# Kernel optimization log

Measured on AMD Instinct MI355X. Metric: run time of the kernel, lower is better.

The kernel has to match this reference:

```python
import jax, jax.numpy as jnp
import numpy as np

B, L, C, EW, H = 4, 512, 512, 64, 8
D = C // H          # dot_dim = 64
NI = 1024           # node ffn inner = round(512*2.0)
EI = 64             # edge ffn inner = round(64*1.0)
CLIP_LO, CLIP_HI = -5.0, 5.0


def _ln(x, g, b):
    m = jnp.mean(x, -1, keepdims=True)
    v = jnp.var(x, -1, keepdims=True)
    return (x - m) * jax.lax.rsqrt(v + 1e-5) * g + b


def setup_inputs() -> dict:
    key = jax.random.key(0)
    ks = iter(jax.random.split(key, 16))
    nrm = lambda shp: (0.02 * jax.random.normal(next(ks), shp)).astype(jnp.float32)
    z = lambda n: jnp.zeros((n,), jnp.float32)
    o = lambda n: jnp.ones((n,), jnp.float32)
    return {
        'h': jax.random.normal(next(ks), (B, L, C), jnp.float32),
        'e': jax.random.normal(next(ks), (B, L, L, EW), jnp.float32),
        'ln_h_g': o(C), 'ln_h_b': z(C),
        'ln_e_g': o(EW), 'ln_e_b': z(EW),
        'W_QKV': nrm((C, 3 * C)), 'b_QKV': z(3 * C),
        'W_E': nrm((EW, H)), 'b_E': z(H),
        'W_G': nrm((EW, H)), 'b_G': z(H),
        'W_Oh': nrm((C, C)), 'b_Oh': z(C),
        'ffn_ln_h_g': o(C), 'ffn_ln_h_b': z(C),
        'W_h1': nrm((C, NI)), 'b_h1': z(NI),
        'W_h2': nrm((NI, C)), 'b_h2': z(C),
        'W_Oe': nrm((H, EW)), 'b_Oe': z(EW),
        'ffn_ln_e_g': o(EW), 'ffn_ln_e_b': z(EW),
        'W_e1': nrm((EW, EI)), 'b_e1': z(EI),
        'W_e2': nrm((EI, EW)), 'b_e2': z(EW),
    }


def reference(h, e, ln_h_g, ln_h_b, ln_e_g, ln_e_b, W_QKV, b_QKV, W_E, b_E,
              W_G, b_G, W_Oh, b_Oh, ffn_ln_h_g, ffn_ln_h_b, W_h1, b_h1,
              W_h2, b_h2, W_Oe, b_Oe, ffn_ln_e_g, ffn_ln_e_b, W_e1, b_e1,
              W_e2, b_e2):
    h_ln = _ln(h, ln_h_g, ln_h_b)
    e_ln = _ln(e, ln_e_g, ln_e_b)
    QKV = h_ln @ W_QKV + b_QKV                    # [B,L,3C]
    E = e_ln @ W_E + b_E                          # [B,L,L,H]
    G = e_ln @ W_G + b_G                          # [B,L,L,H]
    qkv = QKV.reshape(B, L, 3 * D, H)             # torch view(B,L,-1,H)
    Q, K, V = qkv[:, :, :D], qkv[:, :, D:2 * D], qkv[:, :, 2 * D:]
    A_hat = jnp.einsum('bldh,bmdh->blmh', Q, K) * (D ** -0.5)
    H_hat = jnp.clip(A_hat, CLIP_LO, CLIP_HI) + E  # [B,L,L,H]
    gates = jax.nn.sigmoid(G)
    A_tild = jax.nn.softmax(H_hat, axis=2) * gates
    V_att = jnp.einsum('blmh,bmkh->blkh', A_tild, V)  # [B,L,D,H]
    deg = jnp.log1p(jnp.sum(gates, axis=2, keepdims=True))  # [B,L,1,H]
    V_att = (V_att * deg).reshape(B, L, C)
    # node MHA residual + FFN
    h1 = V_att @ W_Oh + b_Oh + h
    h_f = _ln(h1, ffn_ln_h_g, ffn_ln_h_b)
    h_out = h1 + (jax.nn.elu(h_f @ W_h1 + b_h1) @ W_h2 + b_h2)
    # edge MHA residual + FFN
    e1 = H_hat @ W_Oe + b_Oe + e
    e_f = _ln(e1, ffn_ln_e_g, ffn_ln_e_b)
    e_out = e1 + (jax.nn.elu(e_f @ W_e1 + b_e1) @ W_e2 + b_e2)
    return (h_out, e_out)
```

## Files before the change

kernel.cpp:

```cpp
#include <hip/hip_runtime.h>
#include <math.h>

typedef unsigned short u16t;
typedef unsigned int   u32t;
typedef __bf16 bf16x2 __attribute__((ext_vector_type(2)));
typedef __bf16 bf16x8 __attribute__((ext_vector_type(8)));
typedef float  f32x4  __attribute__((ext_vector_type(4)));

#define DEV static __device__ __forceinline__

DEV u16t bfc(float x){ __bf16 b = (__bf16)x; return __builtin_bit_cast(u16t, b); }
DEV u32t pkbf(float a, float b){ bf16x2 v = {(__bf16)a, (__bf16)b}; return __builtin_bit_cast(u32t, v); }
DEV float flc(u16t u){ return __uint_as_float(((u32t)u)<<16); }
DEV u32t pk2(u16t a, u16t b){ return (u32t)a | ((u32t)b<<16); }
DEV f32x4 fz4(){ f32x4 z = {0.f,0.f,0.f,0.f}; return z; }
DEV bf16x8 bz8(){ uint4 z = make_uint4(0u,0u,0u,0u); return __builtin_bit_cast(bf16x8, z); }
DEV f32x4 MFMA(bf16x8 a, bf16x8 b, f32x4 c){ return __builtin_amdgcn_mfma_f32_16x16x32_bf16(a,b,c,0,0,0); }

__global__ void kwTall(const float* __restrict__ A, u16t* __restrict__ oA,
                       const float* __restrict__ B, u16t* __restrict__ oB,
                       const float* __restrict__ C, u16t* __restrict__ oC,
                       const float* __restrict__ D, u16t* __restrict__ oD){
  int id = blockIdx.x*256 + threadIdx.x;
  if (id < 786432){ int n=id>>9, k=id&511; oA[id]=bfc(A[(size_t)k*1536+n]); return; }
  id -= 786432;
  if (id < 262144){ int n=id>>9, k=id&511; int ks=(k&63)*8+(k>>6); oB[id]=bfc(B[(size_t)ks*512+n]); return; }
  id -= 262144;
  if (id < 524288){ int n=id>>9, k=id&511; oC[id]=bfc(C[(size_t)k*1024+n]); return; }
  id -= 524288;
  { int n=id>>10, k=id&1023; oD[id]=bfc(D[(size_t)k*512+n]); }
}

__global__ __launch_bounds__(256) void kln(const float* __restrict__ in, const float* __restrict__ g,
                                           const float* __restrict__ b, u16t* __restrict__ out){
  int wv = threadIdx.x >> 6, lane = threadIdx.x & 63;
  int row = blockIdx.x*4 + wv;
  const float4* rp = reinterpret_cast<const float4*>(in + (size_t)row*512);
  float4 v0 = rp[lane], v1 = rp[lane+64];
  float s = v0.x+v0.y+v0.z+v0.w + v1.x+v1.y+v1.z+v1.w;
  float q = v0.x*v0.x+v0.y*v0.y+v0.z*v0.z+v0.w*v0.w + v1.x*v1.x+v1.y*v1.y+v1.z*v1.z+v1.w*v1.w;
  #pragma unroll
  for (int m=1;m<64;m<<=1){ s += __shfl_xor(s,m); q += __shfl_xor(q,m); }
  float mean = s*(1.f/512.f), var = q*(1.f/512.f)-mean*mean, rs = rsqrtf(var+1e-5f);
  const float4* gp = reinterpret_cast<const float4*>(g);
  const float4* bp = reinterpret_cast<const float4*>(b);
  float4 g0=gp[lane], g1=gp[lane+64], b0=bp[lane], b1=bp[lane+64];
  u16t* op = out + (size_t)row*512;
  uint2 o0, o1;
  o0.x = pkbf((v0.x-mean)*rs*g0.x+b0.x, (v0.y-mean)*rs*g0.y+b0.y);
  o0.y = pkbf((v0.z-mean)*rs*g0.z+b0.z, (v0.w-mean)*rs*g0.w+b0.w);
  o1.x = pkbf((v1.x-mean)*rs*g1.x+b1.x, (v1.y-mean)*rs*g1.y+b1.y);
  o1.y = pkbf((v1.z-mean)*rs*g1.z+b1.z, (v1.w-mean)*rs*g1.w+b1.w);
  reinterpret_cast<uint2*>(op)[lane]    = o0;
  reinterpret_cast<uint2*>(op)[lane+64] = o1;
}

__global__ __launch_bounds__(256) void kqkv(const u16t* __restrict__ hln, const u16t* __restrict__ Wt,
    const float* __restrict__ bias, u16t* __restrict__ Qb, u16t* __restrict__ Kb, u16t* __restrict__ Vt)
{
  __shared__ __align__(16) u16t As[16][520];
  __shared__ __align__(16) u16t Cs[16][1024];
  const int r0 = blockIdx.x*16, t = threadIdx.x;
  const int b8 = (r0 >> 9) * 8, pos0 = r0 & 511;
  {
    int row = t>>4, seg = t&15;
    const uint4* src = reinterpret_cast<const uint4*>(hln + (size_t)(r0+row)*512 + seg*32);
    uint4* dst = reinterpret_cast<uint4*>(&As[row][seg*32]);
    dst[0]=src[0]; dst[1]=src[1]; dst[2]=src[2]; dst[3]=src[3];
  }
  __syncthreads();
  const int wv = t>>6, lane = t&63;
  const int frow = lane&15, kgrp = (lane>>4)*8, rbase = (lane>>4)*4;
  for (int nt=0; nt<24; nt++){
    int n0 = (wv*24+nt)*16;
    f32x4 acc = fz4();
    for (int k0=0;k0<512;k0+=32){
      bf16x8 af = *reinterpret_cast<const bf16x8*>(&As[frow][k0+kgrp]);
      bf16x8 bf_ = *reinterpret_cast<const bf16x8*>(Wt + (size_t)(n0+frow)*512 + k0+kgrp);
      acc = MFMA(af,bf_,acc);
    }
    int col = n0 + frow;
    float bs = bias[col];
    if (n0 < 1024){
      #pragma unroll
      for (int r=0;r<4;r++) Cs[rbase+r][col] = bfc(acc[r]+bs);
    } else {
      int cc = col - 1024, dv = cc>>3, hq = cc&7;
      ushort4 u4 = make_ushort4(bfc(acc[0]+bs), bfc(acc[1]+bs), bfc(acc[2]+bs), bfc(acc[3]+bs));
      *reinterpret_cast<ushort4*>(Vt + ((size_t)(b8+hq)*64 + dv)*512 + pos0 + rbase) = u4;
    }
  }
  __syncthreads();
  {
    int pair = t>>1, halfq = t&1;
    int hq = pair>>4, lq = pair&15, d0 = halfq*32;
    int pos = pos0 + lq;
    u16t* qdst = Qb + ((size_t)(b8+hq)*512 + pos)*64 + d0;
    u16t* kdst = Kb + ((size_t)(b8+hq)*512 + pos)*64 + d0;
    #pragma unroll
    for (int v2=0; v2<4; v2++){
      uint4 u, uk;
      u.x  = pk2(Cs[lq][(d0+v2*8+0)*8+hq], Cs[lq][(d0+v2*8+1)*8+hq]);
      u.y  = pk2(Cs[lq][(d0+v2*8+2)*8+hq], Cs[lq][(d0+v2*8+3)*8+hq]);
      u.z  = pk2(Cs[lq][(d0+v2*8+4)*8+hq], Cs[lq][(d0+v2*8+5)*8+hq]);
      u.w  = pk2(Cs[lq][(d0+v2*8+6)*8+hq], Cs[lq][(d0+v2*8+7)*8+hq]);
      uk.x = pk2(Cs[lq][512+(d0+v2*8+0)*8+hq], Cs[lq][512+(d0+v2*8+1)*8+hq]);
      uk.y = pk2(Cs[lq][512+(d0+v2*8+2)*8+hq], Cs[lq][512+(d0+v2*8+3)*8+hq]);
      uk.z = pk2(Cs[lq][512+(d0+v2*8+4)*8+hq], Cs[lq][512+(d0+v2*8+5)*8+hq]);
      uk.w = pk2(Cs[lq][512+(d0+v2*8+6)*8+hq], Cs[lq][512+(d0+v2*8+7)*8+hq]);
      reinterpret_cast<uint4*>(qdst)[v2] = u;
      reinterpret_cast<uint4*>(kdst)[v2] = uk;
    }
  }
}

__global__ __launch_bounds__(512,4) void kattnF(
    const float* __restrict__ e, const float* __restrict__ lng, const float* __restrict__ lnb,
    const float* __restrict__ WE, const float* __restrict__ bE,
    const float* __restrict__ WG, const float* __restrict__ bG,
    const u16t* __restrict__ Qb, const u16t* __restrict__ Kb, const u16t* __restrict__ Vt,
    const float* __restrict__ WOe, const float* __restrict__ bOe,
    const float* __restrict__ flg, const float* __restrict__ flb,
    const float* __restrict__ We1, const float* __restrict__ be1,
    const float* __restrict__ We2, const float* __restrict__ be2,
    u16t* __restrict__ Vp, float* __restrict__ Sp, float* __restrict__ Dp,
    float* __restrict__ eout)
{
  __shared__ __align__(16) u16t Eln[256][72];
  __shared__ u16t EGb[256][18];
  __shared__ __align__(16) u16t Hl[256][8];
  __shared__ __align__(16) u16t Pgs[16][8][16];
  __shared__ __align__(16) u16t WEGt[16][72];
  __shared__ __align__(16) u16t We1t[64][72];
  __shared__ __align__(16) u16t We2t[64][72];
  __shared__ __align__(16) u16t WOeT[64][8];
  __shared__ float lgs[64], lbs[64], flgs[64], flbs[64], bOes[64], be1s[64], be2s[64];
  __shared__ float bEs[8], bGs[8];

  const int t = threadIdx.x;
  const int b = blockIdx.z, lblk = blockIdx.x, chunk = blockIdx.y;
  const int l0 = lblk*16, m0g = chunk*128, b8 = b*8;

  if (t < 64){
    lgs[t]=lng[t]; lbs[t]=lnb[t]; flgs[t]=flg[t]; flbs[t]=flb[t];
    bOes[t]=bOe[t]; be1s[t]=be1[t]; be2s[t]=be2[t];
  }
  if (t < 8){ bEs[t]=bE[t]; bGs[t]=bG[t]; }
  for (int i=t; i<1024; i+=512){
    int n = i>>6, k = i&63;
    WEGt[n][k] = bfc(n<8 ? WE[k*8+n] : WG[k*8+(n-8)]);
  }
  for (int i=t; i<4096; i+=512){
    int n=i>>6, k=i&63;
    We1t[n][k] = bfc(We1[k*64+n]);
    We2t[n][k] = bfc(We2[k*64+n]);
  }
  {
    int n=t>>3, hh=t&7;
    WOeT[n][hh] = bfc(WOe[hh*64+n]);
  }
  __syncthreads();

  const int wv = t>>6, lane = t&63;
  const int frow = lane&15, kgrp = (lane>>4)*8, rbase = (lane>>4)*4;

  bf16x8 qf[2];
  #pragma unroll
  for (int kk=0;kk<2;kk++)
    qf[kk] = *reinterpret_cast<const bf16x8*>(Qb + ((size_t)(b8+wv)*512 + l0+frow)*64 + kk*32 + kgrp);

  float Ssum[4] = {0.f,0.f,0.f,0.f}, Dsum[4] = {0.f,0.f,0.f,0.f};
  f32x4 accV[4];
  #pragma unroll
  for (int d=0;d<4;d++) accV[d]=fz4();

  const float* ebs[2];
  #pragma unroll
  for (int ti=0; ti<2; ti++)
    ebs[ti] = e + ((size_t)((b*512 + l0 + 2*wv+ti)*512) + m0g + frow)*64 + rbase;

  float4 xr[2][4];
  #pragma unroll
  for (int ti=0; ti<2; ti++)
    #pragma unroll
    for (int nb=0; nb<4; nb++)
      xr[ti][nb] = *reinterpret_cast<const float4*>(ebs[ti] + nb*16);

  #pragma unroll 1
  for (int mt=0; mt<8; mt++){
    const int m0 = m0g + mt*16;
    #pragma unroll
    for (int ti=0; ti<2; ti++){
      const int T = 2*wv + ti;
      float s_=0.f, q_=0.f;
      #pragma unroll
      for (int nb=0; nb<4; nb++){
        float4 v = xr[ti][nb];
        s_ += v.x+v.y+v.z+v.w;
        q_ += v.x*v.x+v.y*v.y+v.z*v.z+v.w*v.w;
      }
      s_ += __shfl_xor(s_,16); q_ += __shfl_xor(q_,16);
      s_ += __shfl_xor(s_,32); q_ += __shfl_xor(q_,32);
      float mean = s_*(1.f/64.f), var = q_*(1.f/64.f)-mean*mean, rs = rsqrtf(var+1e-5f);
      #pragma unroll
      for (int nb=0; nb<4; nb++){
        int n = nb*16 + rbase;
        float4 v = xr[ti][nb];
        uint2 uv;
        uv.x = pkbf((v.x-mean)*rs*lgs[n  ]+lbs[n  ], (v.y-mean)*rs*lgs[n+1]+lbs[n+1]);
        uv.y = pkbf((v.z-mean)*rs*lgs[n+2]+lbs[n+2], (v.w-mean)*rs*lgs[n+3]+lbs[n+3]);
        *reinterpret_cast<uint2*>(&Eln[T*16+frow][n]) = uv;
      }
    }
    #pragma unroll
    for (int ti=0; ti<2; ti++){
      int T = wv*2+ti;
      bf16x8 a0 = *reinterpret_cast<const bf16x8*>(&Eln[T*16+frow][kgrp]);
      bf16x8 a1 = *reinterpret_cast<const bf16x8*>(&Eln[T*16+frow][32+kgrp]);
      bf16x8 w0 = *reinterpret_cast<const bf16x8*>(&WEGt[frow][kgrp]);
      bf16x8 w1 = *reinterpret_cast<const bf16x8*>(&WEGt[frow][32+kgrp]);
      f32x4 acc = fz4(); acc = MFMA(a0,w0,acc); acc = MFMA(a1,w1,acc);
      #pragma unroll
      for (int r=0;r<4;r++) EGb[T*16+rbase+r][frow] = bfc(acc[r]);
    }
    __syncthreads();
    {
      const u16t* kb = Kb + ((size_t)(b8+wv)*512 + m0)*64 + frow*64 + kgrp;
      bf16x8 kf0 = *reinterpret_cast<const bf16x8*>(kb);
      bf16x8 kf1 = *reinterpret_cast<const bf16x8*>(kb + 32);
      f32x4 aq = fz4();
      aq = MFMA(qf[0], kf0, aq);
      aq = MFMA(qf[1], kf1, aq);
      #pragma unroll
      for (int r=0;r<4;r++){
        int lrow = rbase + r;
        int eidx = lrow*16 + frow;
        float ah = aq[r]*0.125f;
        ah = fminf(fmaxf(ah, -5.f), 5.f);
        float Ev = flc(EGb[eidx][wv])   + bEs[wv];
        float Gv = flc(EGb[eidx][8+wv]) + bGs[wv];
        float Hv = ah + Ev;
        float P = __expf(Hv);
        float g = 1.f/(1.f+__expf(-Gv));
        Ssum[r] += P; Dsum[r] += g;
        Hl[eidx][wv] = bfc(Hv);
        Pgs[lrow][wv][frow] = bfc(P*g);
      }
    }
    {
      bf16x8 pa = (kgrp<16)
        ? *reinterpret_cast<const bf16x8*>(&Pgs[frow][wv][kgrp]) : bz8();
      #pragma unroll
      for (int db=0; db<4; db++){
        bf16x8 vb = (kgrp<16)
          ? *reinterpret_cast<const bf16x8*>(Vt + ((size_t)(b8+wv)*64 + db*16+frow)*512 + m0 + kgrp)
          : bz8();
        accV[db] = MFMA(pa, vb, accV[db]);
      }
    }
    __syncthreads();
    #pragma unroll
    for (int ti=0; ti<2; ti++){
      const int T = 2*wv + ti;
      bf16x8 hf_ = bz8();
      if (kgrp==0) hf_ = *reinterpret_cast<const bf16x8*>(&Hl[T*16+frow][0]);
      f32x4 e1a[4];
      #pragma unroll
      for (int nb=0; nb<4; nb++){
        bf16x8 wf = bz8();
        if (kgrp==0) wf = *reinterpret_cast<const bf16x8*>(&WOeT[nb*16][0] + frow*8);
        e1a[nb] = MFMA(wf, hf_, fz4());
      }
      #pragma unroll
      for (int nb=0; nb<4; nb++){
        int n = nb*16 + rbase;
        e1a[nb][0] += bOes[n  ] + xr[ti][nb].x;
        e1a[nb][1] += bOes[n+1] + xr[ti][nb].y;
        e1a[nb][2] += bOes[n+2] + xr[ti][nb].z;
        e1a[nb][3] += bOes[n+3] + xr[ti][nb].w;
      }
      if (mt+1 < 8){
        #pragma unroll
        for (int nb=0; nb<4; nb++)
          xr[ti][nb] = *reinterpret_cast<const float4*>(ebs[ti] + (size_t)(mt+1)*1024 + nb*16);
      }
      {
        float s_=0.f, q_=0.f;
        #pragma unroll
        for (int nb=0; nb<4; nb++){
          #pragma unroll
          for (int r=0;r<4;r++){ float v = e1a[nb][r]; s_ += v; q_ += v*v; }
        }
        s_ += __shfl_xor(s_,16); q_ += __shfl_xor(q_,16);
        s_ += __shfl_xor(s_,32); q_ += __shfl_xor(q_,32);
        float mean = s_*(1.f/64.f), var = q_*(1.f/64.f)-mean*mean, rs = rsqrtf(var+1e-5f);
        #pragma unroll
        for (int nb=0; nb<4; nb++){
          int n = nb*16 + rbase;
          uint2 uv;
          uv.x = pkbf((e1a[nb][0]-mean)*rs*flgs[n  ]+flbs[n  ], (e1a[nb][1]-mean)*rs*flgs[n+1]+flbs[n+1]);
          uv.y = pkbf((e1a[nb][2]-mean)*rs*flgs[n+2]+flbs[n+2], (e1a[nb][3]-mean)*rs*flgs[n+3]+flbs[n+3]);
          *reinterpret_cast<uint2*>(&Eln[T*16+frow][n]) = uv;
        }
      }
      {
        bf16x8 x0 = *reinterpret_cast<const bf16x8*>(&Eln[T*16+frow][kgrp]);
        bf16x8 x1 = *reinterpret_cast<const bf16x8*>(&Eln[T*16+frow][32+kgrp]);
        f32x4 acc1[4];
        #pragma unroll
        for (int nb=0;nb<4;nb++){
          bf16x8 w0 = *reinterpret_cast<const bf16x8*>(&We1t[nb*16+frow][kgrp]);
          bf16x8 w1 = *reinterpret_cast<const bf16x8*>(&We1t[nb*16+frow][32+kgrp]);
          f32x4 a_ = fz4(); a_ = MFMA(w0,x0,a_); a_ = MFMA(w1,x1,a_);
          acc1[nb] = a_;
        }
        #pragma unroll
        for (int nb=0;nb<4;nb++){
          int n = nb*16 + rbase;
          float v0 = acc1[nb][0] + be1s[n  ]; v0 = v0>0.f ? v0 : (__expf(v0)-1.f);
          float v1 = acc1[nb][1] + be1s[n+1]; v1 = v1>0.f ? v1 : (__expf(v1)-1.f);
          float v2 = acc1[nb][2] + be1s[n+2]; v2 = v2>0.f ? v2 : (__expf(v2)-1.f);
          float v3 = acc1[nb][3] + be1s[n+3]; v3 = v3>0.f ? v3 : (__expf(v3)-1.f);
          uint2 uv;
          uv.x = pkbf(v0, v1);
          uv.y = pkbf(v2, v3);
          *reinterpret_cast<uint2*>(&Eln[T*16+frow][n]) = uv;
        }
      }
      {
        bf16x8 x0 = *reinterpret_cast<const bf16x8*>(&Eln[T*16+frow][kgrp]);
        bf16x8 x1 = *reinterpret_cast<const bf16x8*>(&Eln[T*16+frow][32+kgrp]);
        float* eob = eout + ((size_t)((b*512 + l0 + T)*512) + m0 + frow)*64 + rbase;
        #pragma unroll
        for (int nb=0;nb<4;nb++){
          bf16x8 w0 = *reinterpret_cast<const bf16x8*>(&We2t[nb*16+frow][kgrp]);
          bf16x8 w1 = *reinterpret_cast<const bf16x8*>(&We2t[nb*16+frow][32+kgrp]);
          f32x4 a_ = fz4(); a_ = MFMA(w0,x0,a_); a_ = MFMA(w1,x1,a_);
          int n = nb*16 + rbase;
          float4 o;
          o.x = a_[0] + be2s[n  ] + e1a[nb][0];
          o.y = a_[1] + be2s[n+1] + e1a[nb][1];
          o.z = a_[2] + be2s[n+2] + e1a[nb][2];
          o.w = a_[3] + be2s[n+3] + e1a[nb][3];
          *reinterpret_cast<float4*>(eob + nb*16) = o;
        }
      }
    }
  }

  #pragma unroll
  for (int r=0;r<4;r++){
    float sv = Ssum[r], dv = Dsum[r];
    #pragma unroll
    for (int msk=1; msk<16; msk<<=1){ sv += __shfl_xor(sv, msk); dv += __shfl_xor(dv, msk); }
    int lrow = rbase + r;
    if (frow == 0){
      size_t idx = ((size_t)(b*512 + l0 + lrow)*8 + wv)*4 + chunk;
      Sp[idx] = sv; Dp[idx] = dv;
    }
  }
  __syncthreads();
  float* Vo = reinterpret_cast<float*>(&Eln[0][0]);
  #pragma unroll
  for (int db=0; db<4; db++){
    #pragma unroll
    for (int r=0;r<4;r++)
      Vo[(size_t)(rbase+r)*512 + wv*64 + db*16 + frow] = accV[db][r];
  }
  __syncthreads();
  {
    int row = t>>5, i = t&31;
    u16t* vpb = Vp + ((size_t)(chunk*2048 + b*512 + l0 + row))*512 + i*16;
    const float* vsrc = &Vo[(size_t)row*512 + i*16];
    uint4 o0, o1;
    o0.x = pkbf(vsrc[0],  vsrc[1]);  o0.y = pkbf(vsrc[2],  vsrc[3]);
    o0.z = pkbf(vsrc[4],  vsrc[5]);  o0.w = pkbf(vsrc[6],  vsrc[7]);
    o1.x = pkbf(vsrc[8],  vsrc[9]);  o1.y = pkbf(vsrc[10], vsrc[11]);
    o1.z = pkbf(vsrc[12], vsrc[13]); o1.w = pkbf(vsrc[14], vsrc[15]);
    reinterpret_cast<uint4*>(vpb)[0] = o0;
    reinterpret_cast<uint4*>(vpb)[1] = o1;
  }
}

__global__ __launch_bounds__(256) void kvfin(const u16t* __restrict__ Vp,
    const float* __restrict__ Sp, const float* __restrict__ Dp, u16t* __restrict__ Va)
{
  const int row = blockIdx.x;
  const int t = threadIdx.x;
  __shared__ float scl[8];
  if (t < 8){
    const float* sp = Sp + ((size_t)row*8 + t)*4;
    const float* dp = Dp + ((size_t)row*8 + t)*4;
    float S = sp[0]+sp[1]+sp[2]+sp[3];
    float D = dp[0]+dp[1]+dp[2]+dp[3];
    scl[t] = log1pf(D)/S;
  }
  __syncthreads();
  int c = t*2;
  float v0=0.f, v1=0.f;
  #pragma unroll
  for (int ch=0; ch<4; ch++){
    u32t u = *reinterpret_cast<const u32t*>(Vp + ((size_t)(ch*2048 + row))*512 + c);
    v0 += flc((u16t)(u & 0xffffu));
    v1 += flc((u16t)(u >> 16));
  }
  float s = scl[c>>6];
  *reinterpret_cast<u32t*>(Va + (size_t)row*512 + c) = pkbf(v0*s, v1*s);
}

__global__ __launch_bounds__(256) void kgemmNS(const u16t* __restrict__ A, const u16t* __restrict__ Bt,
    const float* __restrict__ bias, const float* __restrict__ res,
    float* __restrict__ outf, u16t* __restrict__ outb, int N, int K, int do_elu)
{
  __shared__ __align__(16) u16t As[16][1032];
  const int r0 = blockIdx.x*16, t = threadIdx.x;
  {
    int row = t>>4, seg = t&15, cnt = K>>4;
    const uint4* src = reinterpret_cast<const uint4*>(A + (size_t)(r0+row)*K + seg*cnt);
    uint4* dst = reinterpret_cast<uint4*>(&As[row][seg*cnt]);
    for (int i=0;i<(cnt>>3);i++) dst[i] = src[i];
  }
  __syncthreads();
  const int wv = t>>6, lane = t&63;
  const int frow = lane&15, kgrp = (lane>>4)*8, rbase = (lane>>4)*4;
  int n0 = (blockIdx.y*4 + wv)*16;
  f32x4 acc = fz4();
  for (int k0=0;k0<K;k0+=32){
    bf16x8 af = *reinterpret_cast<const bf16x8*>(&As[frow][k0+kgrp]);
    bf16x8 bf_ = *reinterpret_cast<const bf16x8*>(Bt + (size_t)(n0+frow)*K + k0+kgrp);
    acc = MFMA(af,bf_,acc);
  }
  int col = n0 + frow;
  float bs = bias[col];
  #pragma unroll
  for (int r=0;r<4;r++){
    size_t row = (size_t)(r0 + rbase + r);
    float v = acc[r] + bs;
    if (do_elu) v = v>0.f ? v : (__expf(v)-1.f);
    if (res)  v += res[row*N + col];
    if (outf) outf[row*N + col] = v;
    if (outb) outb[row*N + col] = bfc(v);
  }
}

extern "C" void kernel_launch(void* const* d_in, const int* in_sizes, int n_in,
                              void* d_out, int out_size, void* d_ws, size_t ws_size,
                              hipStream_t stream)
{
  (void)in_sizes; (void)n_in; (void)out_size; (void)ws_size;
  const float* h      = (const float*)d_in[0];
  const float* e      = (const float*)d_in[1];
  const float* ln_h_g = (const float*)d_in[2];
  const float* ln_h_b = (const float*)d_in[3];
  const float* ln_e_g = (const float*)d_in[4];
  const float* ln_e_b = (const float*)d_in[5];
  const float* W_QKV  = (const float*)d_in[6];
  const float* b_QKV  = (const float*)d_in[7];
  const float* W_E    = (const float*)d_in[8];
  const float* b_E    = (const float*)d_in[9];
  const float* W_G    = (const float*)d_in[10];
  const float* b_G    = (const float*)d_in[11];
  const float* W_Oh   = (const float*)d_in[12];
  const float* b_Oh   = (const float*)d_in[13];
  const float* f_ln_h_g = (const float*)d_in[14];
  const float* f_ln_h_b = (const float*)d_in[15];
  const float* W_h1   = (const float*)d_in[16];
  const float* b_h1   = (const float*)d_in[17];
  const float* W_h2   = (const float*)d_in[18];
  const float* b_h2   = (const float*)d_in[19];
  const float* W_Oe   = (const float*)d_in[20];
  const float* b_Oe   = (const float*)d_in[21];
  const float* f_ln_e_g = (const float*)d_in[22];
  const float* f_ln_e_b = (const float*)d_in[23];
  const float* W_e1   = (const float*)d_in[24];
  const float* b_e1   = (const float*)d_in[25];
  const float* W_e2   = (const float*)d_in[26];
  const float* b_e2   = (const float*)d_in[27];

  float* out   = (float*)d_out;
  float* h_out = out;
  float* e_out = out + (size_t)4*512*512;

  char* w = (char*)d_ws;
  size_t off = 0;
  auto alloc = [&](size_t bytes)->char*{ char* p = w + off; off += (bytes + 255) & ~(size_t)255; return p; };
  u16t* hln   = (u16t*)alloc(2048ull*512*2);
  u16t* WtQKV = (u16t*)alloc(1536ull*512*2);
  u16t* WtOh  = (u16t*)alloc(512ull*512*2);
  u16t* WtH1  = (u16t*)alloc(1024ull*512*2);
  u16t* WtH2  = (u16t*)alloc(512ull*1024*2);
  u16t* Qb    = (u16t*)alloc(4ull*8*512*64*2);
  u16t* Kb    = (u16t*)alloc(4ull*8*512*64*2);
  u16t* Vt    = (u16t*)alloc(4ull*8*64*512*2);
  u16t* Vp    = (u16t*)alloc(4ull*2048*512*2);
  float* Sp   = (float*)alloc(4ull*512*8*4*4);
  float* Dp   = (float*)alloc(4ull*512*8*4*4);
  u16t* Va    = (u16t*)alloc(2048ull*512*2);
  float* h1   = (float*)alloc(2048ull*512*4);
  u16t* hfb   = (u16t*)alloc(2048ull*512*2);
  u16t* U     = (u16t*)alloc(2048ull*1024*2);

  kwTall<<<8192, 256, 0, stream>>>(W_QKV, WtQKV, W_Oh, WtOh, W_h1, WtH1, W_h2, WtH2);
  kln<<<512, 256, 0, stream>>>(h, ln_h_g, ln_h_b, hln);
  kqkv<<<128, 256, 0, stream>>>(hln, WtQKV, b_QKV, Qb, Kb, Vt);
  kattnF<<<dim3(32,4,4), 512, 0, stream>>>(e, ln_e_g, ln_e_b, W_E, b_E, W_G, b_G,
      Qb, Kb, Vt, W_Oe, b_Oe, f_ln_e_g, f_ln_e_b, W_e1, b_e1, W_e2, b_e2,
      Vp, Sp, Dp, e_out);
  kvfin<<<2048, 256, 0, stream>>>(Vp, Sp, Dp, Va);
  kgemmNS<<<dim3(128,8), 256, 0, stream>>>(Va, WtOh, b_Oh, h, h1, nullptr, 512, 512, 0);
  kln<<<512, 256, 0, stream>>>(h1, f_ln_h_g, f_ln_h_b, hfb);
  kgemmNS<<<dim3(128,16), 256, 0, stream>>>(hfb, WtH1, b_h1, nullptr, nullptr, U, 1024, 512, 1);
  kgemmNS<<<dim3(128,8), 256, 0, stream>>>(U, WtH2, b_h2, h1, h_out, nullptr, 512, 1024, 0);
}
```

Measured before the change: 383.8 us.

## Fuse node tail into one kernel, merge prep kernels, prefetch K/V fragments

```diff
diff --git a/kernel.cpp b/kernel.cpp
--- a/kernel.cpp
+++ b/kernel.cpp
@@ -17,11 +17,37 @@
 DEV bf16x8 bz8(){ uint4 z = make_uint4(0u,0u,0u,0u); return __builtin_bit_cast(bf16x8, z); }
 DEV f32x4 MFMA(bf16x8 a, bf16x8 b, f32x4 c){ return __builtin_amdgcn_mfma_f32_16x16x32_bf16(a,b,c,0,0,0); }
 
-__global__ void kwTall(const float* __restrict__ A, u16t* __restrict__ oA,
-                       const float* __restrict__ B, u16t* __restrict__ oB,
-                       const float* __restrict__ C, u16t* __restrict__ oC,
-                       const float* __restrict__ D, u16t* __restrict__ oD){
-  int id = blockIdx.x*256 + threadIdx.x;
+__global__ __launch_bounds__(256) void kprep(
+    const float* __restrict__ h, const float* __restrict__ g, const float* __restrict__ bb, u16t* __restrict__ hln,
+    const float* __restrict__ A, u16t* __restrict__ oA,
+    const float* __restrict__ B, u16t* __restrict__ oB,
+    const float* __restrict__ C, u16t* __restrict__ oC,
+    const float* __restrict__ D, u16t* __restrict__ oD)
+{
+  if (blockIdx.x < 512){
+    int wv = threadIdx.x >> 6, lane = threadIdx.x & 63;
+    int row = blockIdx.x*4 + wv;
+    const float4* rp = reinterpret_cast<const float4*>(h + (size_t)row*512);
+    float4 v0 = rp[lane], v1 = rp[lane+64];
+    float s = v0.x+v0.y+v0.z+v0.w + v1.x+v1.y+v1.z+v1.w;
+    float q = v0.x*v0.x+v0.y*v0.y+v0.z*v0.z+v0.w*v0.w + v1.x*v1.x+v1.y*v1.y+v1.z*v1.z+v1.w*v1.w;
+    #pragma unroll
+    for (int m=1;m<64;m<<=1){ s += __shfl_xor(s,m); q += __shfl_xor(q,m); }
+    float mean = s*(1.f/512.f), var = q*(1.f/512.f)-mean*mean, rs = rsqrtf(var+1e-5f);
+    const float4* gp = reinterpret_cast<const float4*>(g);
+    const float4* bp = reinterpret_cast<const float4*>(bb);
+    float4 g0=gp[lane], g1=gp[lane+64], b0=bp[lane], b1=bp[lane+64];
+    u16t* op = hln + (size_t)row*512;
+    uint2 o0, o1;
+    o0.x = pkbf((v0.x-mean)*rs*g0.x+b0.x, (v0.y-mean)*rs*g0.y+b0.y);
+    o0.y = pkbf((v0.z-mean)*rs*g0.z+b0.z, (v0.w-mean)*rs*g0.w+b0.w);
+    o1.x = pkbf((v1.x-mean)*rs*g1.x+b1.x, (v1.y-mean)*rs*g1.y+b1.y);
+    o1.y = pkbf((v1.z-mean)*rs*g1.z+b1.z, (v1.w-mean)*rs*g1.w+b1.w);
+    reinterpret_cast<uint2*>(op)[lane]    = o0;
+    reinterpret_cast<uint2*>(op)[lane+64] = o1;
+    return;
+  }
+  int id = (blockIdx.x-512)*256 + threadIdx.x;
   if (id < 786432){ int n=id>>9, k=id&511; oA[id]=bfc(A[(size_t)k*1536+n]); return; }
   id -= 786432;
   if (id < 262144){ int n=id>>9, k=id&511; int ks=(k&63)*8+(k>>6); oB[id]=bfc(B[(size_t)ks*512+n]); return; }
@@ -29,30 +55,6 @@
   if (id < 524288){ int n=id>>9, k=id&511; oC[id]=bfc(C[(size_t)k*1024+n]); return; }
   id -= 524288;
   { int n=id>>10, k=id&1023; oD[id]=bfc(D[(size_t)k*512+n]); }
-}
-
-__global__ __launch_bounds__(256) void kln(const float* __restrict__ in, const float* __restrict__ g,
-                                           const float* __restrict__ b, u16t* __restrict__ out){
-  int wv = threadIdx.x >> 6, lane = threadIdx.x & 63;
-  int row = blockIdx.x*4 + wv;
-  const float4* rp = reinterpret_cast<const float4*>(in + (size_t)row*512);
-  float4 v0 = rp[lane], v1 = rp[lane+64];
-  float s = v0.x+v0.y+v0.z+v0.w + v1.x+v1.y+v1.z+v1.w;
-  float q = v0.x*v0.x+v0.y*v0.y+v0.z*v0.z+v0.w*v0.w + v1.x*v1.x+v1.y*v1.y+v1.z*v1.z+v1.w*v1.w;
-  #pragma unroll
-  for (int m=1;m<64;m<<=1){ s += __shfl_xor(s,m); q += __shfl_xor(q,m); }
-  float mean = s*(1.f/512.f), var = q*(1.f/512.f)-mean*mean, rs = rsqrtf(var+1e-5f);
-  const float4* gp = reinterpret_cast<const float4*>(g);
-  const float4* bp = reinterpret_cast<const float4*>(b);
-  float4 g0=gp[lane], g1=gp[lane+64], b0=bp[lane], b1=bp[lane+64];
-  u16t* op = out + (size_t)row*512;
-  uint2 o0, o1;
-  o0.x = pkbf((v0.x-mean)*rs*g0.x+b0.x, (v0.y-mean)*rs*g0.y+b0.y);
-  o0.y = pkbf((v0.z-mean)*rs*g0.z+b0.z, (v0.w-mean)*rs*g0.w+b0.w);
-  o1.x = pkbf((v1.x-mean)*rs*g1.x+b1.x, (v1.y-mean)*rs*g1.y+b1.y);
-  o1.y = pkbf((v1.z-mean)*rs*g1.z+b1.z, (v1.w-mean)*rs*g1.w+b1.w);
-  reinterpret_cast<uint2*>(op)[lane]    = o0;
-  reinterpret_cast<uint2*>(op)[lane+64] = o1;
 }
 
 __global__ __launch_bounds__(256) void kqkv(const u16t* __restrict__ hln, const u16t* __restrict__ Wt,
@@ -186,6 +188,18 @@
     for (int nb=0; nb<4; nb++)
       xr[ti][nb] = *reinterpret_cast<const float4*>(ebs[ti] + nb*16);
 
+  bf16x8 kfc[2], vfc[4];
+  {
+    const u16t* kb = Kb + ((size_t)(b8+wv)*512 + m0g)*64 + frow*64 + kgrp;
+    kfc[0] = *reinterpret_cast<const bf16x8*>(kb);
+    kfc[1] = *reinterpret_cast<const bf16x8*>(kb + 32);
+    #pragma unroll
+    for (int db=0; db<4; db++)
+      vfc[db] = (kgrp<16)
+        ? *reinterpret_cast<const bf16x8*>(Vt + ((size_t)(b8+wv)*64 + db*16+frow)*512 + m0g + kgrp)
+        : bz8();
+  }
+
   #pragma unroll 1
   for (int mt=0; mt<8; mt++){
     const int m0 = m0g + mt*16;
@@ -225,12 +239,9 @@
     }
     __syncthreads();
     {
-      const u16t* kb = Kb + ((size_t)(b8+wv)*512 + m0)*64 + frow*64 + kgrp;
-      bf16x8 kf0 = *reinterpret_cast<const bf16x8*>(kb);
-      bf16x8 kf1 = *reinterpret_cast<const bf16x8*>(kb + 32);
       f32x4 aq = fz4();
-      aq = MFMA(qf[0], kf0, aq);
-      aq = MFMA(qf[1], kf1, aq);
+      aq = MFMA(qf[0], kfc[0], aq);
+      aq = MFMA(qf[1], kfc[1], aq);
       #pragma unroll
       for (int r=0;r<4;r++){
         int lrow = rbase + r;
@@ -251,12 +262,19 @@
       bf16x8 pa = (kgrp<16)
         ? *reinterpret_cast<const bf16x8*>(&Pgs[frow][wv][kgrp]) : bz8();
       #pragma unroll
-      for (int db=0; db<4; db++){
-        bf16x8 vb = (kgrp<16)
-          ? *reinterpret_cast<const bf16x8*>(Vt + ((size_t)(b8+wv)*64 + db*16+frow)*512 + m0 + kgrp)
+      for (int db=0; db<4; db++)
+        accV[db] = MFMA(pa, vfc[db], accV[db]);
+    }
+    if (mt+1 < 8){
+      const int mn = m0 + 16;
+      const u16t* kb = Kb + ((size_t)(b8+wv)*512 + mn)*64 + frow*64 + kgrp;
+      kfc[0] = *reinterpret_cast<const bf16x8*>(kb);
+      kfc[1] = *reinterpret_cast<const bf16x8*>(kb + 32);
+      #pragma unroll
+      for (int db=0; db<4; db++)
+        vfc[db] = (kgrp<16)
+          ? *reinterpret_cast<const bf16x8*>(Vt + ((size_t)(b8+wv)*64 + db*16+frow)*512 + mn + kgrp)
           : bz8();
-        accV[db] = MFMA(pa, vb, accV[db]);
-      }
     }
     __syncthreads();
     #pragma unroll
@@ -382,64 +400,135 @@
   }
 }
 
-__global__ __launch_bounds__(256) void kvfin(const u16t* __restrict__ Vp,
-    const float* __restrict__ Sp, const float* __restrict__ Dp, u16t* __restrict__ Va)
+__global__ __launch_bounds__(512) void khp(
+    const u16t* __restrict__ Vp, const float* __restrict__ Sp, const float* __restrict__ Dp,
+    const float* __restrict__ h,
+    const u16t* __restrict__ WtOh, const float* __restrict__ bOh,
+    const float* __restrict__ lg, const float* __restrict__ lb,
+    const u16t* __restrict__ WtH1, const float* __restrict__ bh1,
+    const u16t* __restrict__ WtH2, const float* __restrict__ bh2,
+    float* __restrict__ hout)
 {
-  const int row = blockIdx.x;
+  __shared__ __align__(16) u16t As[16][520];
+  __shared__ __align__(16) float H1[8][516];
+  __shared__ __align__(16) u16t Ub[16][1040];
+  __shared__ float scl[8][8];
   const int t = threadIdx.x;
-  __shared__ float scl[8];
-  if (t < 8){
-    const float* sp = Sp + ((size_t)row*8 + t)*4;
-    const float* dp = Dp + ((size_t)row*8 + t)*4;
+  const int r0 = blockIdx.x*8;
+  {
+    uint4 z = make_uint4(0,0,0,0);
+    for (int i=t; i<8*65; i+=512){ int row=8+i/65, c=i%65; reinterpret_cast<uint4*>(&As[row][0])[c] = z; }
+    for (int i=t; i<8*130; i+=512){ int row=8+i/130, c=i%130; reinterpret_cast<uint4*>(&Ub[row][0])[c] = z; }
+  }
+  if (t < 64){
+    int row = t>>3, hq = t&7;
+    const float* sp = Sp + ((size_t)(r0+row)*8 + hq)*4;
+    const float* dp = Dp + ((size_t)(r0+row)*8 + hq)*4;
     float S = sp[0]+sp[1]+sp[2]+sp[3];
     float D = dp[0]+dp[1]+dp[2]+dp[3];
-    scl[t] = log1pf(D)/S;
-  }
-  __syncthreads();
-  int c = t*2;
-  float v0=0.f, v1=0.f;
-  #pragma unroll
-  for (int ch=0; ch<4; ch++){
-    u32t u = *reinterpret_cast<const u32t*>(Vp + ((size_t)(ch*2048 + row))*512 + c);
-    v0 += flc((u16t)(u & 0xffffu));
-    v1 += flc((u16t)(u >> 16));
-  }
-  float s = scl[c>>6];
-  *reinterpret_cast<u32t*>(Va + (size_t)row*512 + c) = pkbf(v0*s, v1*s);
-}
-
-__global__ __launch_bounds__(256) void kgemmNS(const u16t* __restrict__ A, const u16t* __restrict__ Bt,
-    const float* __restrict__ bias, const float* __restrict__ res,
-    float* __restrict__ outf, u16t* __restrict__ outb, int N, int K, int do_elu)
-{
-  __shared__ __align__(16) u16t As[16][1032];
-  const int r0 = blockIdx.x*16, t = threadIdx.x;
-  {
-    int row = t>>4, seg = t&15, cnt = K>>4;
-    const uint4* src = reinterpret_cast<const uint4*>(A + (size_t)(r0+row)*K + seg*cnt);
-    uint4* dst = reinterpret_cast<uint4*>(&As[row][seg*cnt]);
-    for (int i=0;i<(cnt>>3);i++) dst[i] = src[i];
+    scl[row][hq] = log1pf(D)/S;
+  }
+  __syncthreads();
+  {
+    int row = t>>6, i = t&63;
+    float acc[8];
+    #pragma unroll
+    for (int j=0;j<8;j++) acc[j]=0.f;
+    #pragma unroll
+    for (int ch=0; ch<4; ch++){
+      uint4 u = *reinterpret_cast<const uint4*>(Vp + ((size_t)(ch*2048 + r0 + row))*512 + i*8);
+      const u32t* uu = reinterpret_cast<const u32t*>(&u);
+      #pragma unroll
+      for (int j=0;j<4;j++){
+        acc[j*2]   += flc((u16t)(uu[j]&0xffffu));
+        acc[j*2+1] += flc((u16t)(uu[j]>>16));
+      }
+    }
+    float s = scl[row][i>>3];
+    uint4 o;
+    o.x = pkbf(acc[0]*s, acc[1]*s);
+    o.y = pkbf(acc[2]*s, acc[3]*s);
+    o.z = pkbf(acc[4]*s, acc[5]*s);
+    o.w = pkbf(acc[6]*s, acc[7]*s);
+    *reinterpret_cast<uint4*>(&As[row][i*8]) = o;
   }
   __syncthreads();
   const int wv = t>>6, lane = t&63;
   const int frow = lane&15, kgrp = (lane>>4)*8, rbase = (lane>>4)*4;
-  int n0 = (blockIdx.y*4 + wv)*16;
-  f32x4 acc = fz4();
-  for (int k0=0;k0<K;k0+=32){
-    bf16x8 af = *reinterpret_cast<const bf16x8*>(&As[frow][k0+kgrp]);
-    bf16x8 bf_ = *reinterpret_cast<const bf16x8*>(Bt + (size_t)(n0+frow)*K + k0+kgrp);
-    acc = MFMA(af,bf_,acc);
-  }
-  int col = n0 + frow;
-  float bs = bias[col];
-  #pragma unroll
-  for (int r=0;r<4;r++){
-    size_t row = (size_t)(r0 + rbase + r);
-    float v = acc[r] + bs;
-    if (do_elu) v = v>0.f ? v : (__expf(v)-1.f);
-    if (res)  v += res[row*N + col];
-    if (outf) outf[row*N + col] = v;
-    if (outb) outb[row*N + col] = bfc(v);
+  #pragma unroll 1
+  for (int nt=0; nt<4; nt++){
+    int n0 = (nt*8+wv)*16;
+    f32x4 acc = fz4();
+    for (int k0=0;k0<512;k0+=32){
+      bf16x8 af = *reinterpret_cast<const bf16x8*>(&As[frow][k0+kgrp]);
+      bf16x8 bf_ = *reinterpret_cast<const bf16x8*>(WtOh + (size_t)(n0+frow)*512 + k0+kgrp);
+      acc = MFMA(af,bf_,acc);
+    }
+    if (rbase < 8){
+      int col = n0+frow;
+      float bs = bOh[col];
+      #pragma unroll
+      for (int r=0;r<4;r++){
+        int row = rbase+r;
+        H1[row][col] = acc[r] + bs + h[(size_t)(r0+row)*512 + col];
+      }
+    }
+  }
+  __syncthreads();
+  {
+    int row = t>>6, i = t&63;
+    float s_=0.f, q_=0.f;
+    #pragma unroll
+    for (int j=0;j<8;j++){ float v = H1[row][i*8+j]; s_+=v; q_+=v*v; }
+    #pragma unroll
+    for (int m=1;m<64;m<<=1){ s_+=__shfl_xor(s_,m); q_+=__shfl_xor(q_,m); }
+    float mean=s_*(1.f/512.f), var=q_*(1.f/512.f)-mean*mean, rs=rsqrtf(var+1e-5f);
+    #pragma unroll
+    for (int j=0;j<8;j+=2){
+      int c = i*8+j;
+      *reinterpret_cast<u32t*>(&As[row][c]) =
+        pkbf((H1[row][c]-mean)*rs*lg[c]+lb[c], (H1[row][c+1]-mean)*rs*lg[c+1]+lb[c+1]);
+    }
+  }
+  __syncthreads();
+  #pragma unroll 1
+  for (int nt=0; nt<8; nt++){
+    int n0 = (nt*8+wv)*16;
+    f32x4 acc = fz4();
+    for (int k0=0;k0<512;k0+=32){
+      bf16x8 af = *reinterpret_cast<const bf16x8*>(&As[frow][k0+kgrp]);
+      bf16x8 bf_ = *reinterpret_cast<const bf16x8*>(WtH1 + (size_t)(n0+frow)*512 + k0+kgrp);
+      acc = MFMA(af,bf_,acc);
+    }
+    if (rbase < 8){
+      int col = n0+frow;
+      float bs = bh1[col];
+      #pragma unroll
+      for (int r=0;r<4;r++){
+        float v = acc[r]+bs; v = v>0.f?v:(__expf(v)-1.f);
+        Ub[rbase+r][col] = bfc(v);
+      }
+    }
+  }
+  __syncthreads();
+  #pragma unroll 1
+  for (int nt=0; nt<4; nt++){
+    int n0 = (nt*8+wv)*16;
+    f32x4 acc = fz4();
+    for (int k0=0;k0<1024;k0+=32){
+      bf16x8 af = *reinterpret_cast<const bf16x8*>(&Ub[frow][k0+kgrp]);
+      bf16x8 bf_ = *reinterpret_cast<const bf16x8*>(WtH2 + (size_t)(n0+frow)*1024 + k0+kgrp);
+      acc = MFMA(af,bf_,acc);
+    }
+    if (rbase < 8){
+      int col = n0+frow;
+      float bs = bh2[col];
+      #pragma unroll
+      for (int r=0;r<4;r++){
+        int row = rbase+r;
+        hout[(size_t)(r0+row)*512 + col] = acc[r] + bs + H1[row][col];
+      }
+    }
   }
 }
 
@@ -495,20 +584,13 @@
   u16t* Vp    = (u16t*)alloc(4ull*2048*512*2);
   float* Sp   = (float*)alloc(4ull*512*8*4*4);
   float* Dp   = (float*)alloc(4ull*512*8*4*4);
-  u16t* Va    = (u16t*)alloc(2048ull*512*2);
-  float* h1   = (float*)alloc(2048ull*512*4);
-  u16t* hfb   = (u16t*)alloc(2048ull*512*2);
-  u16t* U     = (u16t*)alloc(2048ull*1024*2);
-
-  kwTall<<<8192, 256, 0, stream>>>(W_QKV, WtQKV, W_Oh, WtOh, W_h1, WtH1, W_h2, WtH2);
-  kln<<<512, 256, 0, stream>>>(h, ln_h_g, ln_h_b, hln);
+
+  kprep<<<8704, 256, 0, stream>>>(h, ln_h_g, ln_h_b, hln,
+      W_QKV, WtQKV, W_Oh, WtOh, W_h1, WtH1, W_h2, WtH2);
   kqkv<<<128, 256, 0, stream>>>(hln, WtQKV, b_QKV, Qb, Kb, Vt);
   kattnF<<<dim3(32,4,4), 512, 0, stream>>>(e, ln_e_g, ln_e_b, W_E, b_E, W_G, b_G,
       Qb, Kb, Vt, W_Oe, b_Oe, f_ln_e_g, f_ln_e_b, W_e1, b_e1, W_e2, b_e2,
       Vp, Sp, Dp, e_out);
-  kvfin<<<2048, 256, 0, stream>>>(Vp, Sp, Dp, Va);
-  kgemmNS<<<dim3(128,8), 256, 0, stream>>>(Va, WtOh, b_Oh, h, h1, nullptr, 512, 512, 0);
-  kln<<<512, 256, 0, stream>>>(h1, f_ln_h_g, f_ln_h_b, hfb);
-  kgemmNS<<<dim3(128,16), 256, 0, stream>>>(hfb, WtH1, b_h1, nullptr, nullptr, U, 1024, 512, 1);
-  kgemmNS<<<dim3(128,8), 256, 0, stream>>>(U, WtH2, b_h2, h1, h_out, nullptr, 512, 1024, 0);
+  khp<<<256, 512, 0, stream>>>(Vp, Sp, Dp, h, WtOh, b_Oh, f_ln_h_g, f_ln_h_b,
+      WtH1, b_h1, WtH2, b_h2, h_out);
 }
```

Result: slower. 490.7 us (+27.8%).
